# Kernel optimization log

Hardware: AMD Instinct MI355X
Metric: run time of the kernel (lower is better)

## Reference

```python
import jax, jax.numpy as jnp
import numpy as np

M, K, D = 8, 4096, 512  # groups, codes per group, total dim
DG = D // M             # per-group dim = 64


def setup_inputs() -> dict:
    key = jax.random.key(0)
    k1, k2, k3 = jax.random.split(key, 3)
    codes = jax.random.randint(k1, (32, 64, 64, M), 0, K, dtype=jnp.int32)
    codebook = jax.random.normal(k2, (M, K, DG), dtype=jnp.float32)
    wv = jax.random.normal(k3, (M, DG, DG), dtype=jnp.float32) / np.sqrt(DG)
    return {"codes": codes, "codebook": codebook, "wv": wv}


def reference(codes, codebook, wv):
    # v[m,k,c] = sum_d codebook[m,k,d] * wv[m,c,d]  (small per-group GEMM)
    v = jnp.einsum('mkd,mcd->mkc', codebook, wv)  # [M, K, DG]
    # one-hot matmul over k is exactly an indexed gather:
    # gathered[n,h,w,m,c] = v[m, codes[n,h,w,m], c]
    m_idx = jnp.arange(v.shape[0])  # [M]
    gathered = v[m_idx[None, None, None, :], codes]  # [n,h,w,M,DG]
    n, h, w = codes.shape[:3]
    out = gathered.reshape(n, h, w, -1)          # [n,h,w,D]
    return jnp.transpose(out, (0, 3, 1, 2))      # [n,D,h,w]
```

## Files before the change

kernel.cpp:

```cpp
#include <hip/hip_runtime.h>
#include <hip/hip_bf16.h>

#define MQ 8
#define KQ 4096
#define DG 64
#define NN 32
#define HW 4096
#define DD 512
#define THW 256
#define TS 33

__global__ __launch_bounds__(256) void compute_v_kernel(
    const float* __restrict__ codebook,
    const float* __restrict__ wv,
    float* __restrict__ v) {
  __shared__ float wv_t[DG][DG + 1];
  __shared__ float cb[64][DG];

  const int m = blockIdx.y;
  const int k0 = blockIdx.x * 64;
  const int tid = threadIdx.x;

  const float4* wvm4 = (const float4*)(wv + (size_t)m * DG * DG);
  for (int i = tid; i < DG * DG / 4; i += 256) {
    int c = i >> 4, d4 = (i & 15) * 4;
    float4 val = wvm4[i];
    wv_t[d4 + 0][c] = val.x;
    wv_t[d4 + 1][c] = val.y;
    wv_t[d4 + 2][c] = val.z;
    wv_t[d4 + 3][c] = val.w;
  }
  const float4* cbm4 = (const float4*)(codebook + ((size_t)m * KQ + k0) * DG);
  float4* cb4 = (float4*)&cb[0][0];
  for (int i = tid; i < 64 * DG / 4; i += 256) cb4[i] = cbm4[i];
  __syncthreads();

  const int c = tid & 63;
  const int kq = tid >> 6;

  float acc[16];
#pragma unroll
  for (int kl = 0; kl < 16; ++kl) acc[kl] = 0.f;

  for (int d4 = 0; d4 < DG; d4 += 4) {
    float w0 = wv_t[d4 + 0][c];
    float w1 = wv_t[d4 + 1][c];
    float w2 = wv_t[d4 + 2][c];
    float w3 = wv_t[d4 + 3][c];
#pragma unroll
    for (int kl = 0; kl < 16; ++kl) {
      float4 cbv = *(const float4*)&cb[kq * 16 + kl][d4];
      acc[kl] += cbv.x * w0 + cbv.y * w1 + cbv.z * w2 + cbv.w * w3;
    }
  }

  float* vout = v + ((size_t)m * KQ + k0) * DG;
#pragma unroll
  for (int kl = 0; kl < 16; ++kl) {
    vout[(size_t)(kq * 16 + kl) * DG + c] = acc[kl];
  }
}

__global__ __launch_bounds__(256) void gather_kernel(
    const int* __restrict__ codes,
    const float* __restrict__ v,
    float* __restrict__ out) {
  __shared__ int scode[THW];
  __shared__ float tile[THW][TS];

  const int b = blockIdx.x;
  const int m = b & 7;
  const int t = b >> 3;
  const int n = t & 31;
  const int hw0 = (t >> 5) * THW;

  const int tid = threadIdx.x;
  const int w = tid >> 6;
  const int l = tid & 63;

  scode[tid] = codes[((size_t)n * HW + hw0 + tid) * MQ + m];
  __syncthreads();

  const float* vm = v + (size_t)m * KQ * DG;
  float* outb = out + ((size_t)n * DD + (size_t)m * DG) * HW + hw0;

#pragma unroll
  for (int ch = 0; ch < 2; ++ch) {
#pragma unroll
    for (int iter = 0; iter < 8; ++iter) {
      int i = iter * 256 + tid;
      int j = i >> 3;
      int bq = i & 7;
      int r = scode[j];
      float4 val = *(const float4*)(vm + (size_t)r * DG + ch * 32 + bq * 4);
      tile[j][bq * 4 + 0] = val.x;
      tile[j][bq * 4 + 1] = val.y;
      tile[j][bq * 4 + 2] = val.z;
      tile[j][bq * 4 + 3] = val.w;
    }
    __syncthreads();

#pragma unroll
    for (int u = 0; u < 8; ++u) {
      int cc = w * 8 + u;
      int c = ch * 32 + cc;
#pragma unroll
      for (int q = 0; q < 4; ++q) {
        int j = q * 64 + l;
        __builtin_nontemporal_store(tile[j][cc],
                                    outb + (size_t)c * HW + j);
      }
    }
    __syncthreads();
  }
}

extern "C" void kernel_launch(void* const* d_in, const int* in_sizes, int n_in,
                              void* d_out, int out_size, void* d_ws, size_t ws_size,
                              hipStream_t stream) {
  const int* codes = (const int*)d_in[0];
  const float* codebook = (const float*)d_in[1];
  const float* wv = (const float*)d_in[2];
  float* out = (float*)d_out;
  float* v = (float*)d_ws;

  compute_v_kernel<<<dim3(64, 8), 256, 0, stream>>>(codebook, wv, v);
  gather_kernel<<<NN * MQ * (HW / THW), 256, 0, stream>>>(codes, v, out);
}
```

Baseline: 302.7 us.

## Stage per-group 4-channel slice of v in LDS as lookup table for gather

The gather kernel is restructured so each block loads a 4-channel slice of v for all 4096 codes of one group into LDS (64 KB), then processes 8 images. Each thread reads 4 consecutive codes and looks up LDS entries, transposing them in registers into float4 nontemporal stores along hw. This removes the per-tile global gather of v rows and the shared-memory transpose tile with its syncs. In exchange, codes are re-read 16 times (once per channel slice) with strided scalar loads, LDS lookups are random and may hit bank conflicts, and the grid shrinks to 512 blocks.

```diff
diff --git a/kernel.cpp b/kernel.cpp
--- a/kernel.cpp
+++ b/kernel.cpp
@@ -1,5 +1,4 @@
 #include <hip/hip_runtime.h>
-#include <hip/hip_bf16.h>
 
 #define MQ 8
 #define KQ 4096
@@ -7,8 +6,8 @@
 #define NN 32
 #define HW 4096
 #define DD 512
-#define THW 256
-#define TS 33
+
+typedef float f32x4 __attribute__((ext_vector_type(4)));
 
 __global__ __launch_bounds__(256) void compute_v_kernel(
     const float* __restrict__ codebook,
@@ -61,57 +60,59 @@
   }
 }
 
-__global__ __launch_bounds__(256) void gather_kernel(
+__global__ __launch_bounds__(512, 4) void gather_lut_kernel(
     const int* __restrict__ codes,
     const float* __restrict__ v,
     float* __restrict__ out) {
-  __shared__ int scode[THW];
-  __shared__ float tile[THW][TS];
+  __shared__ f32x4 lut[KQ];
 
   const int b = blockIdx.x;
   const int m = b & 7;
-  const int t = b >> 3;
-  const int n = t & 31;
-  const int hw0 = (t >> 5) * THW;
+  const int rest = b >> 3;
+  const int cq = rest & 15;
+  const int n0 = (rest >> 4) * 8;
 
   const int tid = threadIdx.x;
   const int w = tid >> 6;
   const int l = tid & 63;
 
-  scode[tid] = codes[((size_t)n * HW + hw0 + tid) * MQ + m];
+  const float* vm = v + (size_t)m * KQ * DG + cq * 4;
+#pragma unroll
+  for (int i = 0; i < 8; ++i) {
+    int k = i * 512 + tid;
+    lut[k] = *(const f32x4*)(vm + (size_t)k * DG);
+  }
   __syncthreads();
 
-  const float* vm = v + (size_t)m * KQ * DG;
-  float* outb = out + ((size_t)n * DD + (size_t)m * DG) * HW + hw0;
+  for (int i = 0; i < 8; ++i) {
+    const int n = n0 + i;
+    const int* cp = codes + (size_t)n * HW * MQ + m;
+    float* ob = out + ((size_t)n * DD + m * DG + cq * 4) * HW;
+
+    int rr[8];
+#pragma unroll
+    for (int q = 0; q < 2; ++q) {
+      const int hwb = (w * 2 + q) * 256 + 4 * l;
+#pragma unroll
+      for (int t = 0; t < 4; ++t) rr[q * 4 + t] = cp[(size_t)(hwb + t) * MQ];
+    }
 
 #pragma unroll
-  for (int ch = 0; ch < 2; ++ch) {
-#pragma unroll
-    for (int iter = 0; iter < 8; ++iter) {
-      int i = iter * 256 + tid;
-      int j = i >> 3;
-      int bq = i & 7;
-      int r = scode[j];
-      float4 val = *(const float4*)(vm + (size_t)r * DG + ch * 32 + bq * 4);
-      tile[j][bq * 4 + 0] = val.x;
-      tile[j][bq * 4 + 1] = val.y;
-      tile[j][bq * 4 + 2] = val.z;
-      tile[j][bq * 4 + 3] = val.w;
+    for (int q = 0; q < 2; ++q) {
+      const int hwb = (w * 2 + q) * 256 + 4 * l;
+      f32x4 v0 = lut[rr[q * 4 + 0]];
+      f32x4 v1 = lut[rr[q * 4 + 1]];
+      f32x4 v2 = lut[rr[q * 4 + 2]];
+      f32x4 v3 = lut[rr[q * 4 + 3]];
+      f32x4 o0 = {v0.x, v1.x, v2.x, v3.x};
+      f32x4 o1 = {v0.y, v1.y, v2.y, v3.y};
+      f32x4 o2 = {v0.z, v1.z, v2.z, v3.z};
+      f32x4 o3 = {v0.w, v1.w, v2.w, v3.w};
+      __builtin_nontemporal_store(o0, (f32x4*)(ob + 0 * HW + hwb));
+      __builtin_nontemporal_store(o1, (f32x4*)(ob + 1 * HW + hwb));
+      __builtin_nontemporal_store(o2, (f32x4*)(ob + 2 * HW + hwb));
+      __builtin_nontemporal_store(o3, (f32x4*)(ob + 3 * HW + hwb));
     }
-    __syncthreads();
-
-#pragma unroll
-    for (int u = 0; u < 8; ++u) {
-      int cc = w * 8 + u;
-      int c = ch * 32 + cc;
-#pragma unroll
-      for (int q = 0; q < 4; ++q) {
-        int j = q * 64 + l;
-        __builtin_nontemporal_store(tile[j][cc],
-                                    outb + (size_t)c * HW + j);
-      }
-    }
-    __syncthreads();
   }
 }
 
@@ -125,5 +126,5 @@
   float* v = (float*)d_ws;
 
   compute_v_kernel<<<dim3(64, 8), 256, 0, stream>>>(codebook, wv, v);
-  gather_kernel<<<NN * MQ * (HW / THW), 256, 0, stream>>>(codes, v, out);
+  gather_lut_kernel<<<MQ * 16 * (NN / 8), 512, 0, stream>>>(codes, v, out);
 }
```

Result: slower. 329.0 us (+8.7%).
